# Performance work log

Measured on AMD Instinct MI355X. Metric: run time of the kernel, lower is better.

Reference implementation:

```python
import jax, jax.numpy as jnp
import numpy as np
from jax import lax

B, C, H, W = 2, 128, 128, 128
Hs, Ws = 64, 64
DG, KK = 8, 9          # deformable groups, kernel positions (3x3)
CG = C // DG           # channels per deformable group = 16
COUT = C // 2          # dcn output channels = 64


def setup_inputs() -> dict:
    key = jax.random.key(0)
    ks = jax.random.split(key, 9)
    s = 0.05
    return {
        "feat_l": jax.random.normal(ks[0], (B, C, H, W), jnp.float32),
        "feat_s": jax.random.normal(ks[1], (B, C, Hs, Ws), jnp.float32),
        "fsm_w": jax.random.normal(ks[2], (C, C, 1, 1), jnp.float32) * s,
        "offset_w": jax.random.normal(ks[3], (C, 2 * C, 1, 1), jnp.float32) * s,
        "com_w": jax.random.normal(ks[4], (3 * DG * KK, C, 3, 3), jnp.float32) * s,
        "com_b": jax.random.normal(ks[5], (3 * DG * KK,), jnp.float32) * s,
        "dcn_w": jax.random.normal(ks[6], (COUT, C, 3, 3), jnp.float32) * s,
        "dcn_b": jax.random.normal(ks[7], (COUT,), jnp.float32) * s,
        "cat_w": jax.random.normal(ks[8], (C, COUT, 1, 1), jnp.float32) * s,
    }


def _conv(x, w, pad):
    return lax.conv_general_dilated(x, w, (1, 1), [(pad, pad), (pad, pad)],
                                    dimension_numbers=("NCHW", "OIHW", "NCHW"))


def _bilinear(feat_g, py, px):
    # feat_g: [B,DG,CG,H,W]; py/px: [B,DG,KK,H,W] fractional sample coords.
    Hf, Wf = feat_g.shape[-2], feat_g.shape[-1]
    y0 = jnp.floor(py)
    x0 = jnp.floor(px)
    ly = py - y0
    lx = px - x0
    y0i = y0.astype(jnp.int32)
    x0i = x0.astype(jnp.int32)
    flat = feat_g.reshape(B, DG, 1, CG, Hf * Wf)  # broadcast over KK

    def gather(yi, xi, wgt):
        valid = ((yi >= 0) & (yi < Hf) & (xi >= 0) & (xi < Wf)).astype(feat_g.dtype)
        idx = (jnp.clip(yi, 0, Hf - 1) * Wf + jnp.clip(xi, 0, Wf - 1))
        idx = idx.reshape(B, DG, KK, 1, H * W)
        v = jnp.take_along_axis(flat, idx, axis=-1)  # [B,DG,KK,CG,H*W]
        return v * (wgt * valid).reshape(B, DG, KK, 1, H * W)

    acc = (gather(y0i, x0i, (1 - ly) * (1 - lx))
           + gather(y0i, x0i + 1, (1 - ly) * lx)
           + gather(y0i + 1, x0i, ly * (1 - lx))
           + gather(y0i + 1, x0i + 1, ly * lx))
    return acc.reshape(B, DG, KK, CG, H, W)


def reference(feat_l, feat_s, fsm_w, offset_w, com_w, com_b, dcn_w, dcn_b, cat_w):
    # nearest-neighbor upsample of feat_s to feat_l's HxW (F.interpolate nearest)
    idx_h = (jnp.arange(H) * Hs) // H
    idx_w = (jnp.arange(W) * Ws) // W
    feat_up = feat_s[:, :, idx_h][:, :, :, idx_w]

    feat_arm = jax.nn.relu(_conv(feat_l, fsm_w, 0))                       # FSM (1x1 conv+relu)
    off_feat = jax.nn.relu(_conv(jnp.concatenate([feat_arm, feat_up * 2], axis=1), offset_w, 0))

    # DCNv2 pack: 3x3 conv -> (o1, o2, mask)
    om = _conv(off_feat, com_w, 1) + com_b[None, :, None, None]
    o1, o2, m = jnp.split(om, 3, axis=1)
    offset = jnp.concatenate([o1, o2], axis=1).reshape(B, DG, KK, 2, H, W)  # (y,x) per (g,pos)
    mask = jax.nn.sigmoid(m).reshape(B, DG, KK, H, W)

    # sampling coords: p + kernel offset + learned offset (stride=1, pad=1, dil=1)
    kyy = (jnp.arange(KK) // 3 - 1).astype(jnp.float32)
    kxx = (jnp.arange(KK) % 3 - 1).astype(jnp.float32)
    py = (jnp.arange(H, dtype=jnp.float32)[None, None, None, :, None]
          + kyy[None, None, :, None, None] + offset[:, :, :, 0])
    px = (jnp.arange(W, dtype=jnp.float32)[None, None, None, None, :]
          + kxx[None, None, :, None, None] + offset[:, :, :, 1])

    feat_g = feat_up.reshape(B, DG, CG, H, W)
    val = _bilinear(feat_g, py, px) * mask[:, :, :, None]  # [B,DG,KK,CG,H,W]

    w_r = dcn_w.reshape(COUT, DG, CG, KK)
    out = jnp.einsum('bgkchw,ogck->bohw', val, w_r) + dcn_b[None, :, None, None]
    feat_align = jax.nn.relu(out)

    return jax.nn.relu(_conv(feat_align, cat_w, 0)) + feat_arm
```

## Files before the change

### kernel.cpp

```cpp
#include <hip/hip_runtime.h>
#include <cstdint>
#include <cstddef>


typedef _Float16 f16x8 __attribute__((ext_vector_type(8)));
typedef _Float16 f16x4 __attribute__((ext_vector_type(4)));
typedef float    f32x4 __attribute__((ext_vector_type(4)));

__device__ __forceinline__ float relu_(float x) { return fmaxf(x, 0.f); }

template<int MODE, int CIN>
__global__ __launch_bounds__(256) void conv1x1_kernel(
    const float* __restrict__ in1, const float* __restrict__ in2,
    const float* __restrict__ Wm, float* __restrict__ out)
{
  constexpr int IN1C = (MODE == 2) ? 64 : 128;
  const int b  = blockIdx.y;
  const int p0 = blockIdx.x * 64;
  const int tid = threadIdx.x;
  const int tx = tid & 7;
  const int ty = tid >> 3;

  __shared__ float Xs[16][64];
  __shared__ float Wt[16][128];

  float acc[4][8];
#pragma unroll
  for (int i = 0; i < 4; ++i)
#pragma unroll
    for (int j = 0; j < 8; ++j) acc[i][j] = 0.f;

  const int cS  = tid >> 4;
  const int pxS = (tid & 15) * 4;
  const int ocS = (tid & 15) * 8;

  for (int cc = 0; cc < CIN; cc += 16) {
    __syncthreads();
    {
      int gc = cc + cS;
      float4 v;
      if (MODE == 1 && gc >= 128) {
        int sc = gc - 128;
        float t[4];
#pragma unroll
        for (int j = 0; j < 4; ++j) {
          int pp = p0 + pxS + j;
          int hh = pp >> 7, ww = pp & 127;
          t[j] = 2.f * in2[((size_t)(b * 128 + sc) << 12) + ((hh >> 1) << 6) + (ww >> 1)];
        }
        v = make_float4(t[0], t[1], t[2], t[3]);
      } else {
        v = *(const float4*)(in1 + ((size_t)(b * IN1C + gc) << 14) + p0 + pxS);
      }
      *(float4*)&Xs[cS][pxS] = v;
#pragma unroll
      for (int j = 0; j < 8; ++j)
        Wt[cS][ocS + j] = Wm[(ocS + j) * CIN + cc + cS];
    }
    __syncthreads();
#pragma unroll
    for (int c = 0; c < 16; ++c) {
      float4 wv = *(const float4*)&Wt[c][ty * 4];
      float4 x0 = *(const float4*)&Xs[c][tx * 8];
      float4 x1 = *(const float4*)&Xs[c][tx * 8 + 4];
      float xs[8] = {x0.x, x0.y, x0.z, x0.w, x1.x, x1.y, x1.z, x1.w};
      float wf[4] = {wv.x, wv.y, wv.z, wv.w};
#pragma unroll
      for (int i = 0; i < 4; ++i)
#pragma unroll
        for (int j = 0; j < 8; ++j)
          acc[i][j] = fmaf(wf[i], xs[j], acc[i][j]);
    }
  }

#pragma unroll
  for (int i = 0; i < 4; ++i) {
    int oc = ty * 4 + i;
    size_t base = ((size_t)(b * 128 + oc) << 14) + p0 + tx * 8;
    float r[8];
#pragma unroll
    for (int j = 0; j < 8; ++j) r[j] = relu_(acc[i][j]);
    if (MODE == 2) {
#pragma unroll
      for (int j = 0; j < 8; ++j) r[j] += in2[base + j];
    }
    *(float4*)(out + base)     = make_float4(r[0], r[1], r[2], r[3]);
    *(float4*)(out + base + 4) = make_float4(r[4], r[5], r[6], r[7]);
  }
}

__global__ __launch_bounds__(256) void t2h2_kernel(
    const float* __restrict__ fl, const float* __restrict__ fs,
    _Float16* __restrict__ flTh, _Float16* __restrict__ fsTh)
{
  const int bx = blockIdx.x;
  const float* src;
  _Float16* dst;
  int HW, p0;
  if (bx < 512) { src = fl; dst = flTh; HW = 16384; p0 = bx * 32; }
  else          { src = fs; dst = fsTh; HW = 4096;  p0 = (bx - 512) * 32; }
  const int b  = blockIdx.z;
  const int c0 = blockIdx.y * 32;
  const int tid = threadIdx.x;
  __shared__ float T[32][33];
  {
    int pxl = tid & 31, cy = tid >> 5;
#pragma unroll
    for (int j = 0; j < 4; ++j) {
      int c = cy + j * 8;
      T[c][pxl] = src[((size_t)(b * 128 + c0 + c)) * HW + p0 + pxl];
    }
  }
  __syncthreads();
  {
    int cq = tid & 7, pr = tid >> 3;
    f16x4 v;
#pragma unroll
    for (int e = 0; e < 4; ++e) v[e] = (_Float16)T[cq * 4 + e][pr];
    *(f16x4*)&dst[(((size_t)b * HW) + p0 + pr) * 128 + c0 + cq * 4] = v;
  }
}

__global__ __launch_bounds__(256) void wfall_kernel(
    const float* __restrict__ fsm_w, const float* __restrict__ offset_w,
    const float* __restrict__ com_w, const float* __restrict__ dcn_w,
    const float* __restrict__ cat_w,
    _Float16* __restrict__ WfA, _Float16* __restrict__ WfB,
    _Float16* __restrict__ WfP, _Float16* __restrict__ Wf2,
    _Float16* __restrict__ WfC)
{
  const int bid = blockIdx.x;
  if (bid < 8) {
    int idx = bid * 256 + threadIdx.x;
    int lane = idx & 63;
    int t = idx >> 6;
    int m = t & 7, q = t >> 3;
    int oc = m * 16 + (lane & 15);
    int c0 = q * 32 + (lane >> 4) * 8;
    f16x8 v;
#pragma unroll
    for (int j = 0; j < 8; ++j) v[j] = (_Float16)fsm_w[oc * 128 + c0 + j];
    ((f16x8*)WfA)[idx] = v;
  } else if (bid < 24) {
    int idx = (bid - 8) * 256 + threadIdx.x;
    int lane = idx & 63;
    int t = idx >> 6;
    int m = t & 7, q = t >> 3;
    int oc = m * 16 + (lane & 15);
    int c0 = q * 32 + (lane >> 4) * 8;
    float s = (q >= 4) ? 2.f : 1.f;
    f16x8 v;
#pragma unroll
    for (int j = 0; j < 8; ++j) v[j] = (_Float16)(offset_w[oc * 256 + c0 + j] * s);
    ((f16x8*)WfB)[idx] = v;
  } else if (bid < 168) {
    int idx = (bid - 24) * 256 + threadIdx.x;
    int lane = idx & 63;
    int t = idx >> 6;
    int m = t & 7;
    int t2 = t >> 3;
    int half = t2 & 1, q = t2 >> 1;
    int kk = q >> 2;
    int ic0 = (q & 3) * 32 + (lane >> 4) * 8;
    int oc = half * 128 + m * 16 + (lane & 15);
    f16x8 v;
#pragma unroll
    for (int j = 0; j < 8; ++j) {
      float x = (oc < 216) ? com_w[((size_t)oc * 128 + ic0 + j) * 9 + kk] : 0.f;
      v[j] = (_Float16)x;
    }
    ((f16x8*)WfP)[idx] = v;
  } else if (bid < 204) {
    int idx = (bid - 168) * 256 + threadIdx.x;
    int lane = idx & 63;
    int t = idx >> 6;
    int m = t & 3, q = t >> 2;
    int oc = m * 16 + (lane & 15);
    f16x8 v;
#pragma unroll
    for (int j = 0; j < 8; ++j) {
      int rp = q * 32 + (lane >> 4) * 8 + j;
      int c = rp & 15, tt = rp >> 4;
      int g = tt / 9, k = tt % 9;
      v[j] = (_Float16)dcn_w[((size_t)oc * 128 + g * 16 + c) * 9 + k];
    }
    ((f16x8*)Wf2)[idx] = v;
  } else {
    int idx = (bid - 204) * 256 + threadIdx.x;
    int lane = idx & 63;
    int t = idx >> 6;
    int m = t & 7, q = t >> 3;
    int oc = m * 16 + (lane & 15);
    int k0 = q * 32 + (lane >> 4) * 8;
    f16x8 v;
#pragma unroll
    for (int j = 0; j < 8; ++j) v[j] = (_Float16)cat_w[oc * 64 + k0 + j];
    ((f16x8*)WfC)[idx] = v;
  }
}

__global__ __launch_bounds__(256) void fsm_gemm_kernel(
    const _Float16* __restrict__ flTh, const _Float16* __restrict__ WfA,
    float* __restrict__ arm, _Float16* __restrict__ armh)
{
  const int b    = blockIdx.y;
  const int tid  = threadIdx.x;
  const int wv   = tid >> 6;
  const int lane = tid & 63;
  const int px0  = blockIdx.x * 64 + wv * 16;
  const int pxl  = px0 + (lane & 15);

  f32x4 acc[8];
#pragma unroll
  for (int m = 0; m < 8; ++m) acc[m] = (f32x4){0.f, 0.f, 0.f, 0.f};

  const f16x8* Bp = (const f16x8*)flTh + (((size_t)b << 14) + pxl) * 16 + (lane >> 4);
  const f16x8* Ap = (const f16x8*)WfA + lane;

#pragma unroll
  for (int q = 0; q < 4; ++q) {
    f16x8 bf = Bp[q * 4];
#pragma unroll
    for (int m = 0; m < 8; ++m)
      acc[m] = __builtin_amdgcn_mfma_f32_16x16x32_f16(Ap[(q * 8 + m) * 64], bf, acc[m], 0, 0, 0);
  }

  const int r0 = (lane >> 4) * 4;
#pragma unroll
  for (int m = 0; m < 8; ++m) {
    f16x4 h;
#pragma unroll
    for (int r = 0; r < 4; ++r) {
      float v = relu_(acc[m][r]);
      arm[((size_t)(b * 128 + m * 16 + r0 + r) << 14) + pxl] = v;
      h[r] = (_Float16)v;
    }
    *(f16x4*)&armh[(((size_t)b << 14) + pxl) * 128 + m * 16 + r0] = h;
  }
}

__global__ __launch_bounds__(256) void off_gemm_kernel(
    const _Float16* __restrict__ armh, const _Float16* __restrict__ fsTh,
    const _Float16* __restrict__ WfB, _Float16* __restrict__ offh)
{
  const int b    = blockIdx.y;
  const int tid  = threadIdx.x;
  const int wv   = tid >> 6;
  const int lane = tid & 63;
  const int px0  = blockIdx.x * 64 + wv * 16;
  const int pxl  = px0 + (lane & 15);
  const int h = pxl >> 7, w = pxl & 127;
  const int pup = ((h >> 1) << 6) + (w >> 1);

  f32x4 acc[8];
#pragma unroll
  for (int m = 0; m < 8; ++m) acc[m] = (f32x4){0.f, 0.f, 0.f, 0.f};

  const f16x8* BpA = (const f16x8*)armh + (((size_t)b << 14) + pxl) * 16 + (lane >> 4);
  const f16x8* BpU = (const f16x8*)fsTh + (((size_t)b << 12) + pup) * 16 + (lane >> 4);
  const f16x8* Ap  = (const f16x8*)WfB + lane;

#pragma unroll
  for (int q = 0; q < 8; ++q) {
    f16x8 bf = (q < 4) ? BpA[q * 4] : BpU[(q - 4) * 4];
#pragma unroll
    for (int m = 0; m < 8; ++m)
      acc[m] = __builtin_amdgcn_mfma_f32_16x16x32_f16(Ap[(q * 8 + m) * 64], bf, acc[m], 0, 0, 0);
  }

  const int r0 = (lane >> 4) * 4;
#pragma unroll
  for (int m = 0; m < 8; ++m) {
    f16x4 hh;
#pragma unroll
    for (int r = 0; r < 4; ++r) hh[r] = (_Float16)relu_(acc[m][r]);
    *(f16x4*)&offh[(((size_t)b << 14) + pxl) * 128 + m * 16 + r0] = hh;
  }
}

__global__ __launch_bounds__(256) void com_gemm_kernel(
    const _Float16* __restrict__ offh, const _Float16* __restrict__ WfP,
    const float* __restrict__ cb, float* __restrict__ om)
{
  const int b    = blockIdx.z;
  const int half = blockIdx.y;
  const int tid  = threadIdx.x;
  const int lane = tid & 63;
  const int px0  = blockIdx.x * 64 + (tid >> 6) * 16;
  const int pxl  = px0 + (lane & 15);
  const int h = pxl >> 7, w = pxl & 127;

  __shared__ f16x8 As[512];

  f32x4 acc[8];
#pragma unroll
  for (int m = 0; m < 8; ++m) acc[m] = (f32x4){0.f, 0.f, 0.f, 0.f};

  const f16x8* Bbase = (const f16x8*)offh + ((size_t)b << 14) * 16 + (lane >> 4);
  const f16x8* Wp    = (const f16x8*)WfP + half * 512 + tid * 2;
  const f16x8 zero = {(_Float16)0.f, (_Float16)0.f, (_Float16)0.f, (_Float16)0.f,
                      (_Float16)0.f, (_Float16)0.f, (_Float16)0.f, (_Float16)0.f};

  auto loadB = [&](int t) -> f16x8 {
    const int kk = t >> 2, ic4 = t & 3;
    const int hh = h + kk / 3 - 1;
    const int ww = w + kk % 3 - 1;
    const bool valid = ((unsigned)hh < 128u) && ((unsigned)ww < 128u);
    const int ps = valid ? ((hh << 7) + ww) : 0;
    f16x8 bf = Bbase[(size_t)ps * 16 + ic4 * 4];
    return valid ? bf : zero;
  };

  f16x8 rA0 = Wp[0], rA1 = Wp[1];
  f16x8 bfA = loadB(0), bfB = loadB(1);

#pragma unroll 1
  for (int tt = 0; tt < 18; ++tt) {
    const int t0 = tt * 2;
    __syncthreads();
    As[tid * 2] = rA0; As[tid * 2 + 1] = rA1;
    __syncthreads();
    rA0 = Wp[(t0 + 1) * 1024]; rA1 = Wp[(t0 + 1) * 1024 + 1];
    {
      f16x8 bu = bfA;
      if (t0 + 2 < 36) bfA = loadB(t0 + 2);
#pragma unroll
      for (int m = 0; m < 8; ++m)
        acc[m] = __builtin_amdgcn_mfma_f32_16x16x32_f16(As[m * 64 + lane], bu, acc[m], 0, 0, 0);
    }
    __syncthreads();
    As[tid * 2] = rA0; As[tid * 2 + 1] = rA1;
    __syncthreads();
    if (t0 + 2 < 36) { rA0 = Wp[(t0 + 2) * 1024]; rA1 = Wp[(t0 + 2) * 1024 + 1]; }
    {
      f16x8 bu = bfB;
      if (t0 + 3 < 36) bfB = loadB(t0 + 3);
#pragma unroll
      for (int m = 0; m < 8; ++m)
        acc[m] = __builtin_amdgcn_mfma_f32_16x16x32_f16(As[m * 64 + lane], bu, acc[m], 0, 0, 0);
    }
  }

  const int r0i = (lane >> 4) * 4;
#pragma unroll
  for (int m = 0; m < 8; ++m) {
#pragma unroll
    for (int r = 0; r < 4; ++r) {
      int oc = half * 128 + m * 16 + r0i + r;
      if (oc < 216)
        om[((size_t)(b * 216 + oc) << 14) + pxl] = acc[m][r] + cb[oc];
    }
  }
}

__global__ __launch_bounds__(256) void dcn_fused_kernel(
    const _Float16* __restrict__ fsTh, const float* __restrict__ om,
    const _Float16* __restrict__ Wf2, const float* __restrict__ db,
    _Float16* __restrict__ alh)
{
  const int b    = blockIdx.y;
  const int tid  = threadIdx.x;
  const int wv   = tid >> 6;
  const int lane = tid & 63;
  const int px0  = blockIdx.x * 64 + wv * 16;
  const int pxl  = px0 + (lane & 15);
  const int h = pxl >> 7, w = pxl & 127;
  const int t9add = lane >> 5;
  const int chalf = ((lane >> 4) & 1) << 3;

  const float* omp = om + (((size_t)b * 216) << 14) + pxl;
  const _Float16* fb = fsTh + ((size_t)b << 19);
  const f16x8* Ap = (const f16x8*)Wf2 + lane;

  f32x4 acc[4];
#pragma unroll
  for (int m = 0; m < 4; ++m) acc[m] = (f32x4){0.f, 0.f, 0.f, 0.f};

#pragma unroll 1
  for (int q = 0; q < 36; ++q) {
    const int t9 = 2 * q + t9add;
    const int g = t9 / 9;
    const int k = t9 - g * 9;

    const float offy = omp[(size_t)(g * 18 + 2 * k) << 14];
    const float offx = omp[(size_t)(g * 18 + 2 * k + 1) << 14];
    const float mraw = omp[(size_t)(144 + t9) << 14];
    const float mv = 1.f / (1.f + __expf(-mraw));

    const float py  = (float)(h + k / 3 - 1) + offy;
    const float pxx = (float)(w + k % 3 - 1) + offx;
    const float y0f = floorf(py), x0f = floorf(pxx);
    const float ly = py - y0f, lx = pxx - x0f;
    const int y0 = (int)y0f, x0i = (int)x0f;
    const int y1 = y0 + 1, x1 = x0i + 1;

    const int y0c = min(max(y0, 0), 127), y1c = min(max(y1, 0), 127);
    const int x0c = min(max(x0i, 0), 127), x1c = min(max(x1, 0), 127);

    float w00 = (1.f - ly) * (1.f - lx) * mv;
    float w01 = (1.f - ly) * lx * mv;
    float w10 = ly * (1.f - lx) * mv;
    float w11 = ly * lx * mv;
    const bool vy0 = (unsigned)y0 < 128u, vy1 = (unsigned)y1 < 128u;
    const bool vx0 = (unsigned)x0i < 128u, vx1 = (unsigned)x1 < 128u;
    w00 = (vy0 && vx0) ? w00 : 0.f;
    w01 = (vy0 && vx1) ? w01 : 0.f;
    w10 = (vy1 && vx0) ? w10 : 0.f;
    w11 = (vy1 && vx1) ? w11 : 0.f;

    const int gb = g * 16 + chalf;
    const int a00 = ((((y0c >> 1) << 6) + (x0c >> 1)) << 7) + gb;
    const int a01 = ((((y0c >> 1) << 6) + (x1c >> 1)) << 7) + gb;
    const int a10 = ((((y1c >> 1) << 6) + (x0c >> 1)) << 7) + gb;
    const int a11 = ((((y1c >> 1) << 6) + (x1c >> 1)) << 7) + gb;

    f16x8 t00 = *(const f16x8*)(fb + a00);
    f16x8 t01 = *(const f16x8*)(fb + a01);
    f16x8 t10 = *(const f16x8*)(fb + a10);
    f16x8 t11 = *(const f16x8*)(fb + a11);

    f16x8 bf;
#pragma unroll
    for (int j = 0; j < 8; ++j)
      bf[j] = (_Float16)(w00 * (float)t00[j] + w01 * (float)t01[j]
                       + w10 * (float)t10[j] + w11 * (float)t11[j]);

    const f16x8* ap = Ap + q * 256;
#pragma unroll
    for (int m = 0; m < 4; ++m)
      acc[m] = __builtin_amdgcn_mfma_f32_16x16x32_f16(ap[m * 64], bf, acc[m], 0, 0, 0);
  }

  const int r0 = (lane >> 4) * 4;
#pragma unroll
  for (int m = 0; m < 4; ++m) {
    f16x4 hv;
#pragma unroll
    for (int r = 0; r < 4; ++r) {
      int oc = m * 16 + r0 + r;
      hv[r] = (_Float16)relu_(acc[m][r] + db[oc]);
    }
    *(f16x4*)&alh[(((size_t)b << 14) + pxl) * 64 + m * 16 + r0] = hv;
  }
}

__global__ __launch_bounds__(256) void cat_gemm_kernel(
    const _Float16* __restrict__ alh, const _Float16* __restrict__ WfC,
    const float* __restrict__ arm, float* __restrict__ out)
{
  const int b    = blockIdx.y;
  const int tid  = threadIdx.x;
  const int wv   = tid >> 6;
  const int lane = tid & 63;
  const int px0  = blockIdx.x * 64 + wv * 16;
  const int pxl  = px0 + (lane & 15);

  f32x4 acc[8];
#pragma unroll
  for (int m = 0; m < 8; ++m) acc[m] = (f32x4){0.f, 0.f, 0.f, 0.f};

  const f16x8* Bp = (const f16x8*)alh + (((size_t)b << 14) + pxl) * 8 + (lane >> 4);
  const f16x8* Ap = (const f16x8*)WfC + lane;

#pragma unroll
  for (int q = 0; q < 2; ++q) {
    f16x8 bf = Bp[q * 4];
#pragma unroll
    for (int m = 0; m < 8; ++m)
      acc[m] = __builtin_amdgcn_mfma_f32_16x16x32_f16(Ap[(q * 8 + m) * 64], bf, acc[m], 0, 0, 0);
  }

  const int r0 = (lane >> 4) * 4;
#pragma unroll
  for (int m = 0; m < 8; ++m) {
#pragma unroll
    for (int r = 0; r < 4; ++r) {
      int oc = m * 16 + r0 + r;
      size_t a = ((size_t)(b * 128 + oc) << 14) + pxl;
      out[a] = relu_(acc[m][r]) + arm[a];
    }
  }
}

__global__ __launch_bounds__(256) void com_conv_kernel(
    const float* __restrict__ x, const float* __restrict__ cw,
    const float* __restrict__ cb, float* __restrict__ om)
{
  const int b    = blockIdx.z;
  const int ocg  = blockIdx.y;
  const int tile = blockIdx.x;
  const int th = (tile >> 2) * 32, tw = (tile & 3) * 32;
  const int tid = threadIdx.x;
  const int lw = (tid & 7) * 4;
  const int lh = tid >> 3;

  __shared__ float Xs[8 * 34 * 34];

  float acc[8][4];
#pragma unroll
  for (int a = 0; a < 8; ++a)
#pragma unroll
    for (int p = 0; p < 4; ++p) acc[a][p] = 0.f;

  for (int cc = 0; cc < 128; cc += 8) {
    __syncthreads();
    for (int idx = tid; idx < 8 * 1156; idx += 256) {
      int ic  = idx / 1156;
      int rem = idx - ic * 1156;
      int yy  = rem / 34;
      int xx  = rem - yy * 34;
      int gh = th + yy - 1, gw = tw + xx - 1;
      float v = 0.f;
      if ((unsigned)gh < 128u && (unsigned)gw < 128u)
        v = x[((size_t)(b * 128 + cc + ic) << 14) + (gh << 7) + gw];
      Xs[idx] = v;
    }
    __syncthreads();
#pragma unroll 1
    for (int ic = 0; ic < 8; ++ic) {
      float xr[3][6];
#pragma unroll
      for (int ky = 0; ky < 3; ++ky)
#pragma unroll
        for (int xx = 0; xx < 6; ++xx)
          xr[ky][xx] = Xs[ic * 1156 + (lh + ky) * 34 + lw + xx];
      const float* wp = cw + ((size_t)(ocg * 8) * 128 + (cc + ic)) * 9;
#pragma unroll
      for (int a = 0; a < 8; ++a) {
        const float* w9 = wp + a * 1152;
#pragma unroll
        for (int ky = 0; ky < 3; ++ky)
#pragma unroll
          for (int kx = 0; kx < 3; ++kx) {
            float wv = w9[ky * 3 + kx];
#pragma unroll
            for (int p = 0; p < 4; ++p)
              acc[a][p] = fmaf(wv, xr[ky][kx + p], acc[a][p]);
          }
      }
    }
  }

#pragma unroll
  for (int a = 0; a < 8; ++a) {
    int oc = ocg * 8 + a;
    float bv = cb[oc];
    float4 r = make_float4(acc[a][0] + bv, acc[a][1] + bv,
                           acc[a][2] + bv, acc[a][3] + bv);
    *(float4*)(om + ((size_t)(b * 216 + oc) << 14) + ((th + lh) << 7) + tw + lw) = r;
  }
}

__global__ __launch_bounds__(256) void wt_kernel(const float* __restrict__ dw,
                                                 float* __restrict__ wT)
{
  int idx = blockIdx.x * 256 + threadIdx.x;
  int o    = idx & 63;
  int rest = idx >> 6;
  int k    = rest % 9;
  int gc   = rest / 9;
  wT[idx] = dw[(o * 128 + gc) * 9 + k];
}

__global__ __launch_bounds__(256) void dcn_kernel(
    const float* __restrict__ fs, const float* __restrict__ om,
    const float* __restrict__ wT, const float* __restrict__ db,
    float* __restrict__ al)
{
  const int b   = blockIdx.y;
  const int p0  = blockIdx.x * 32;
  const int tid = threadIdx.x;
  const int px  = tid & 31;
  const int g   = tid >> 5;
  const int p = p0 + px;
  const int h = p >> 7, w = p & 127;

  float acc[64];
#pragma unroll
  for (int o = 0; o < 64; ++o) acc[o] = 0.f;

  const size_t omb = ((size_t)b * 216) << 14;
  const float* fsg = fs + (((size_t)(b * 128 + g * 16)) << 12);
  const float* wg  = wT + g * (16 * 9 * 64);

#pragma unroll 1
  for (int k = 0; k < 9; ++k) {
    float offy = om[omb + ((size_t)(g * 18 + 2 * k) << 14) + p];
    float offx = om[omb + ((size_t)(g * 18 + 2 * k + 1) << 14) + p];
    float mraw = om[omb + ((size_t)(144 + g * 9 + k) << 14) + p];
    float mv = 1.f / (1.f + __expf(-mraw));

    float py  = (float)(h + k / 3 - 1) + offy;
    float pxx = (float)(w + k % 3 - 1) + offx;
    float y0f = floorf(py), x0f = floorf(pxx);
    float ly = py - y0f, lx = pxx - x0f;
    int y0 = (int)y0f, x0i = (int)x0f;
    int y1 = y0 + 1, x1 = x0i + 1;

    int y0c = min(max(y0, 0), 127), y1c = min(max(y1, 0), 127);
    int x0c = min(max(x0i, 0), 127), x1c = min(max(x1, 0), 127);
    int ry0 = (y0c >> 1) << 6, ry1 = (y1c >> 1) << 6;
    int cx0 = x0c >> 1, cx1 = x1c >> 1;

    float w00 = (1.f - ly) * (1.f - lx) * mv;
    float w01 = (1.f - ly) * lx * mv;
    float w10 = ly * (1.f - lx) * mv;
    float w11 = ly * lx * mv;
    bool vy0 = (unsigned)y0 < 128u, vy1 = (unsigned)y1 < 128u;
    bool vx0 = (unsigned)x0i < 128u, vx1 = (unsigned)x1 < 128u;
    w00 = (vy0 && vx0) ? w00 : 0.f;
    w01 = (vy0 && vx1) ? w01 : 0.f;
    w10 = (vy1 && vx0) ? w10 : 0.f;
    w11 = (vy1 && vx1) ? w11 : 0.f;

#pragma unroll 1
    for (int c = 0; c < 16; ++c) {
      const float* fc = fsg + (c << 12);
      float v00 = fc[ry0 + cx0];
      float v01 = fc[ry0 + cx1];
      float v10 = fc[ry1 + cx0];
      float v11 = fc[ry1 + cx1];
      float v = w00 * v00 + w01 * v01 + w10 * v10 + w11 * v11;
      const float* wp = wg + (c * 9 + k) * 64;
#pragma unroll
      for (int oq = 0; oq < 16; ++oq) {
        float4 w4 = *(const float4*)(wp + oq * 4);
        acc[oq * 4 + 0] = fmaf(v, w4.x, acc[oq * 4 + 0]);
        acc[oq * 4 + 1] = fmaf(v, w4.y, acc[oq * 4 + 1]);
        acc[oq * 4 + 2] = fmaf(v, w4.z, acc[oq * 4 + 2]);
        acc[oq * 4 + 3] = fmaf(v, w4.w, acc[oq * 4 + 3]);
      }
    }
  }

  __shared__ float red[256][17];
  const int px2 = tid & 31;
  const int og  = tid >> 5;
#pragma unroll
  for (int r = 0; r < 4; ++r) {
    __syncthreads();
#pragma unroll
    for (int j = 0; j < 16; ++j) red[tid][j] = acc[r * 16 + j];
    __syncthreads();
#pragma unroll
    for (int jj = 0; jj < 2; ++jj) {
      int ol = og * 2 + jj;
      float s = 0.f;
#pragma unroll
      for (int gg = 0; gg < 8; ++gg) s += red[gg * 32 + px2][ol];
      int oc = r * 16 + ol;
      s += db[oc];
      al[((size_t)(b * 64 + oc) << 14) + p0 + px2] = fmaxf(s, 0.f);
    }
  }
}

extern "C" void kernel_launch(void* const* d_in, const int* in_sizes, int n_in,
                              void* d_out, int out_size, void* d_ws, size_t ws_size,
                              hipStream_t stream)
{
  const float* feat_l   = (const float*)d_in[0];
  const float* feat_s   = (const float*)d_in[1];
  const float* fsm_w    = (const float*)d_in[2];
  const float* offset_w = (const float*)d_in[3];
  const float* com_w    = (const float*)d_in[4];
  const float* com_b    = (const float*)d_in[5];
  const float* dcn_w    = (const float*)d_in[6];
  const float* dcn_b    = (const float*)d_in[7];
  const float* cat_w    = (const float*)d_in[8];
  float* out = (float*)d_out;
  float* ws  = (float*)d_ws;

  const size_t NEED = (size_t)(4194304 + 7077888 + 2097152 + 1048576 + 37748736) * 4;

  if (ws_size >= NEED) {
    float* arm      = ws;
    float* om       = ws + 4194304;
    _Float16* alh   = (_Float16*)(ws + 11272192);
    _Float16* Wf2   = (_Float16*)(ws + 12320768);
    _Float16* WfC   = (_Float16*)(ws + 12357632);
    _Float16* fsTh  = (_Float16*)(ws + 13369344);
    _Float16* flTh  = (_Float16*)(ws + 13893632);
    _Float16* armh  = (_Float16*)(ws + 15990784);
    _Float16* offh  = (_Float16*)(ws + 18087936);
    _Float16* WfA   = (_Float16*)(ws + 39059456);
    _Float16* WfB   = (_Float16*)(ws + 39067648);
    _Float16* WfP   = (_Float16*)(ws + 39084032);

    hipLaunchKernelGGL(wfall_kernel, dim3(208), dim3(256), 0, stream,
                       fsm_w, offset_w, com_w, dcn_w, cat_w, WfA, WfB, WfP, Wf2, WfC);
    hipLaunchKernelGGL(t2h2_kernel, dim3(640, 4, 2), dim3(256), 0, stream,
                       feat_l, feat_s, flTh, fsTh);
    hipLaunchKernelGGL(fsm_gemm_kernel, dim3(256, 2), dim3(256), 0, stream,
                       flTh, WfA, arm, armh);
    hipLaunchKernelGGL(off_gemm_kernel, dim3(256, 2), dim3(256), 0, stream,
                       armh, fsTh, WfB, offh);
    hipLaunchKernelGGL(com_gemm_kernel, dim3(256, 2, 2), dim3(256), 0, stream,
                       offh, WfP, com_b, om);
    hipLaunchKernelGGL(dcn_fused_kernel, dim3(256, 2), dim3(256), 0, stream,
                       fsTh, om, Wf2, dcn_b, alh);
    hipLaunchKernelGGL(cat_gemm_kernel, dim3(256, 2), dim3(256), 0, stream,
                       alh, WfC, arm, out);
  } else {
    float* arm = ws;
    float* off = ws + 4194304;
    float* om  = ws + 8388608;
    float* al  = ws + 15466496;
    float* wT  = ws + 17563648;

    hipLaunchKernelGGL(wt_kernel, dim3(288), dim3(256), 0, stream, dcn_w, wT);
    hipLaunchKernelGGL((conv1x1_kernel<0, 128>), dim3(256, 2), dim3(256), 0, stream,
                       feat_l, nullptr, fsm_w, arm);
    hipLaunchKernelGGL((conv1x1_kernel<1, 256>), dim3(256, 2), dim3(256), 0, stream,
                       arm, feat_s, offset_w, off);
    hipLaunchKernelGGL(com_conv_kernel, dim3(16, 27, 2), dim3(256), 0, stream,
                       off, com_w, com_b, om);
    hipLaunchKernelGGL(dcn_kernel, dim3(512, 2), dim3(256), 0, stream,
                       feat_s, om, wT, dcn_b, al);
    hipLaunchKernelGGL((conv1x1_kernel<2, 64>), dim3(256, 2), dim3(256), 0, stream,
                       al, arm, cat_w, out);
  }
}
```

Measured before the change: 187.7 us.

## Split DCN reduction over two K-halves with software-pipelined gathers and reduce kernel

The fused DCN kernel is split along the 36-step reduction loop into two halves, one per blockIdx.y, which doubles the grid from 512 to 1024 blocks. Each half writes fp32 partial sums to a workspace buffer, and a new reduce kernel adds the halves, applies bias and ReLU, and stores fp16. Within each half, the offset loads and bilinear corner gathers for the next step are issued before the current step's blend and MFMA, so gather latency is hidden. The cost is an extra launch, 16 MB of partial-sum traffic and higher register pressure.

```diff
diff --git a/kernel.cpp b/kernel.cpp
--- a/kernel.cpp
+++ b/kernel.cpp
@@ -353,12 +353,12 @@
   }
 }
 
-__global__ __launch_bounds__(256) void dcn_fused_kernel(
+__global__ __launch_bounds__(256) void dcn_split_kernel(
     const _Float16* __restrict__ fsTh, const float* __restrict__ om,
-    const _Float16* __restrict__ Wf2, const float* __restrict__ db,
-    _Float16* __restrict__ alh)
-{
-  const int b    = blockIdx.y;
+    const _Float16* __restrict__ Wf2, float* __restrict__ part)
+{
+  const int b    = blockIdx.z;
+  const int kh   = blockIdx.y;
   const int tid  = threadIdx.x;
   const int wv   = tid >> 6;
   const int lane = tid & 63;
@@ -371,77 +371,110 @@
   const float* omp = om + (((size_t)b * 216) << 14) + pxl;
   const _Float16* fb = fsTh + ((size_t)b << 19);
   const f16x8* Ap = (const f16x8*)Wf2 + lane;
+  const int qbeg = kh * 18;
 
   f32x4 acc[4];
 #pragma unroll
   for (int m = 0; m < 4; ++m) acc[m] = (f32x4){0.f, 0.f, 0.f, 0.f};
 
-#pragma unroll 1
-  for (int q = 0; q < 36; ++q) {
+  auto loadOm = [&](int q, float& oy, float& ox, float& mr) {
     const int t9 = 2 * q + t9add;
     const int g = t9 / 9;
     const int k = t9 - g * 9;
-
-    const float offy = omp[(size_t)(g * 18 + 2 * k) << 14];
-    const float offx = omp[(size_t)(g * 18 + 2 * k + 1) << 14];
-    const float mraw = omp[(size_t)(144 + t9) << 14];
-    const float mv = 1.f / (1.f + __expf(-mraw));
-
-    const float py  = (float)(h + k / 3 - 1) + offy;
-    const float pxx = (float)(w + k % 3 - 1) + offx;
+    oy = omp[(size_t)(g * 18 + 2 * k) << 14];
+    ox = omp[(size_t)(g * 18 + 2 * k + 1) << 14];
+    mr = omp[(size_t)(144 + t9) << 14];
+  };
+
+  auto prep = [&](int q, float oy, float ox, float mr,
+                  float& w00, float& w01, float& w10, float& w11,
+                  f16x8& t00, f16x8& t01, f16x8& t10, f16x8& t11) {
+    const int t9 = 2 * q + t9add;
+    const int g = t9 / 9;
+    const int k = t9 - g * 9;
+    const float mv = 1.f / (1.f + __expf(-mr));
+    const float py  = (float)(h + k / 3 - 1) + oy;
+    const float pxx = (float)(w + k % 3 - 1) + ox;
     const float y0f = floorf(py), x0f = floorf(pxx);
     const float ly = py - y0f, lx = pxx - x0f;
     const int y0 = (int)y0f, x0i = (int)x0f;
     const int y1 = y0 + 1, x1 = x0i + 1;
-
     const int y0c = min(max(y0, 0), 127), y1c = min(max(y1, 0), 127);
     const int x0c = min(max(x0i, 0), 127), x1c = min(max(x1, 0), 127);
-
-    float w00 = (1.f - ly) * (1.f - lx) * mv;
-    float w01 = (1.f - ly) * lx * mv;
-    float w10 = ly * (1.f - lx) * mv;
-    float w11 = ly * lx * mv;
+    w00 = (1.f - ly) * (1.f - lx) * mv;
+    w01 = (1.f - ly) * lx * mv;
+    w10 = ly * (1.f - lx) * mv;
+    w11 = ly * lx * mv;
     const bool vy0 = (unsigned)y0 < 128u, vy1 = (unsigned)y1 < 128u;
     const bool vx0 = (unsigned)x0i < 128u, vx1 = (unsigned)x1 < 128u;
     w00 = (vy0 && vx0) ? w00 : 0.f;
     w01 = (vy0 && vx1) ? w01 : 0.f;
     w10 = (vy1 && vx0) ? w10 : 0.f;
     w11 = (vy1 && vx1) ? w11 : 0.f;
-
     const int gb = g * 16 + chalf;
     const int a00 = ((((y0c >> 1) << 6) + (x0c >> 1)) << 7) + gb;
     const int a01 = ((((y0c >> 1) << 6) + (x1c >> 1)) << 7) + gb;
     const int a10 = ((((y1c >> 1) << 6) + (x0c >> 1)) << 7) + gb;
     const int a11 = ((((y1c >> 1) << 6) + (x1c >> 1)) << 7) + gb;
-
-    f16x8 t00 = *(const f16x8*)(fb + a00);
-    f16x8 t01 = *(const f16x8*)(fb + a01);
-    f16x8 t10 = *(const f16x8*)(fb + a10);
-    f16x8 t11 = *(const f16x8*)(fb + a11);
-
+    t00 = *(const f16x8*)(fb + a00);
+    t01 = *(const f16x8*)(fb + a01);
+    t10 = *(const f16x8*)(fb + a10);
+    t11 = *(const f16x8*)(fb + a11);
+  };
+
+  float oyB, oxB, mrB;
+  float w00, w01, w10, w11;
+  f16x8 t00, t01, t10, t11;
+  {
+    float oyA, oxA, mrA;
+    loadOm(qbeg, oyA, oxA, mrA);
+    loadOm(qbeg + 1, oyB, oxB, mrB);
+    prep(qbeg, oyA, oxA, mrA, w00, w01, w10, w11, t00, t01, t10, t11);
+  }
+
+#pragma unroll 1
+  for (int qq = 0; qq < 18; ++qq) {
+    const int q = qbeg + qq;
+    float nw00 = 0.f, nw01 = 0.f, nw10 = 0.f, nw11 = 0.f;
+    f16x8 n00 = t00, n01 = t01, n10 = t10, n11 = t11;
+    if (qq + 1 < 18) {
+      prep(q + 1, oyB, oxB, mrB, nw00, nw01, nw10, nw11, n00, n01, n10, n11);
+      if (qq + 2 < 18) loadOm(q + 2, oyB, oxB, mrB);
+    }
     f16x8 bf;
 #pragma unroll
     for (int j = 0; j < 8; ++j)
       bf[j] = (_Float16)(w00 * (float)t00[j] + w01 * (float)t01[j]
                        + w10 * (float)t10[j] + w11 * (float)t11[j]);
-
     const f16x8* ap = Ap + q * 256;
 #pragma unroll
     for (int m = 0; m < 4; ++m)
       acc[m] = __builtin_amdgcn_mfma_f32_16x16x32_f16(ap[m * 64], bf, acc[m], 0, 0, 0);
+    w00 = nw00; w01 = nw01; w10 = nw10; w11 = nw11;
+    t00 = n00; t01 = n01; t10 = n10; t11 = n11;
   }
 
   const int r0 = (lane >> 4) * 4;
-#pragma unroll
-  for (int m = 0; m < 4; ++m) {
-    f16x4 hv;
-#pragma unroll
-    for (int r = 0; r < 4; ++r) {
-      int oc = m * 16 + r0 + r;
-      hv[r] = (_Float16)relu_(acc[m][r] + db[oc]);
-    }
-    *(f16x4*)&alh[(((size_t)b << 14) + pxl) * 64 + m * 16 + r0] = hv;
-  }
+  float* pp = part + ((size_t)kh << 21) + ((((size_t)b << 14) + pxl) << 6);
+#pragma unroll
+  for (int m = 0; m < 4; ++m)
+    *(f32x4*)(pp + m * 16 + r0) = acc[m];
+}
+
+__global__ __launch_bounds__(256) void dcn_reduce_kernel(
+    const float* __restrict__ part, const float* __restrict__ db,
+    _Float16* __restrict__ alh)
+{
+  const int idx = blockIdx.x * 256 + threadIdx.x;
+  const int oc4 = idx & 15;
+  const size_t base = ((size_t)(idx >> 4) << 6) + oc4 * 4;
+  f32x4 v0 = *(const f32x4*)(part + base);
+  f32x4 v1 = *(const f32x4*)(part + ((size_t)1 << 21) + base);
+  f16x4 hv;
+#pragma unroll
+  for (int r = 0; r < 4; ++r)
+    hv[r] = (_Float16)relu_(v0[r] + v1[r] + db[oc4 * 4 + r]);
+  *(f16x4*)&alh[base] = hv;
 }
 
 __global__ __launch_bounds__(256) void cat_gemm_kernel(
@@ -683,6 +716,7 @@
     _Float16* flTh  = (_Float16*)(ws + 13893632);
     _Float16* armh  = (_Float16*)(ws + 15990784);
     _Float16* offh  = (_Float16*)(ws + 18087936);
+    float*    part  = ws + 20185088;
     _Float16* WfA   = (_Float16*)(ws + 39059456);
     _Float16* WfB   = (_Float16*)(ws + 39067648);
     _Float16* WfP   = (_Float16*)(ws + 39084032);
@@ -697,8 +731,10 @@
                        armh, fsTh, WfB, offh);
     hipLaunchKernelGGL(com_gemm_kernel, dim3(256, 2, 2), dim3(256), 0, stream,
                        offh, WfP, com_b, om);
-    hipLaunchKernelGGL(dcn_fused_kernel, dim3(256, 2), dim3(256), 0, stream,
-                       fsTh, om, Wf2, dcn_b, alh);
+    hipLaunchKernelGGL(dcn_split_kernel, dim3(256, 2, 2), dim3(256), 0, stream,
+                       fsTh, om, Wf2, part);
+    hipLaunchKernelGGL(dcn_reduce_kernel, dim3(2048), dim3(256), 0, stream,
+                       part, dcn_b, alh);
     hipLaunchKernelGGL(cat_gemm_kernel, dim3(256, 2), dim3(256), 0, stream,
                        alh, WfC, arm, out);
   } else {
```

After: 191.8 us. 2.2% more time.
